# Optimization experiments

Measured on AMD Instinct MI355X. Metric: run time of the kernel, lower is better.

Reference implementation:

```python
import jax, jax.numpy as jnp
import numpy as np

TOP_K = 2
ROUTE_SCALE = 1.0
EPS = 1e-20

B, S, D = 2, 512, 1024
E = 8            # num_experts
F = 768          # moe_intermediate_size
FS = 768 * 1     # shared expert intermediate (moe_intermediate_size * num_shared_experts)


def setup_inputs() -> dict:
    key = jax.random.key(0)
    ks = jax.random.split(key, 9)
    s = 0.02
    return {
        "hidden_states": jax.random.normal(ks[0], (B, S, D), dtype=jnp.float32),
        "W_gate_router": jax.random.normal(ks[1], (D, E), dtype=jnp.float32) * s,
        "expert_bias": jnp.zeros((E,), dtype=jnp.float32),
        "Wg": jax.random.normal(ks[2], (E, D, F), dtype=jnp.float32) * s,
        "Wu": jax.random.normal(ks[3], (E, D, F), dtype=jnp.float32) * s,
        "Wd": jax.random.normal(ks[4], (E, F, D), dtype=jnp.float32) * s,
        "Wg_s": jax.random.normal(ks[5], (D, FS), dtype=jnp.float32) * s,
        "Wu_s": jax.random.normal(ks[6], (D, FS), dtype=jnp.float32) * s,
        "Wd_s": jax.random.normal(ks[7], (FS, D), dtype=jnp.float32) * s,
    }


def reference(hidden_states, W_gate_router, expert_bias, Wg, Wu, Wd, Wg_s, Wu_s, Wd_s):
    b, s, d = hidden_states.shape
    x = hidden_states.reshape(-1, d)                      # [T, D]
    T = x.shape[0]

    # ---- token-choice top-k router (sigmoid scoring, route_norm) ----
    logits = x @ W_gate_router                            # [T, E]
    scores = jax.nn.sigmoid(logits.astype(jnp.float32))   # [T, E] fp32
    _, sel = jax.lax.top_k(scores + expert_bias, TOP_K)   # [T, K] (bias only for selection)
    top_scores = jnp.take_along_axis(scores, sel, axis=1)  # [T, K]
    top_scores = top_scores / (top_scores.sum(-1, keepdims=True) + EPS)  # route_norm
    top_scores = top_scores * ROUTE_SCALE

    # ---- shared expert (always active) ----
    shared = (jax.nn.silu(x @ Wg_s) * (x @ Wu_s)) @ Wd_s  # [T, D]

    # ---- dispatch: N = T*K routed slots (scatter-add is order-independent,
    #      so the torch stable-argsort grouping is mathematically a no-op) ----
    tok = jnp.repeat(jnp.arange(T), TOP_K)                # [N] source token per slot
    exp = sel.reshape(-1)                                 # [N] expert per slot
    w = top_scores.reshape(-1)                            # [N]
    xr = x[tok]                                           # [N, D]

    # per-expert SiLU-GLU MLP, vectorized over experts then select own expert's row
    h = jax.nn.silu(jnp.einsum('nd,edf->enf', xr, Wg)) * jnp.einsum('nd,edf->enf', xr, Wu)
    out_all = jnp.einsum('enf,efd->end', h, Wd)           # [E, N, D]
    routed = out_all[exp, jnp.arange(exp.shape[0])]       # [N, D]
    routed = (routed.astype(jnp.float32) * w[:, None]).astype(hidden_states.dtype)

    # ---- combine: scatter-add routed outputs onto shared output ----
    out = shared.at[tok].add(routed)                      # [T, D]
    return out.reshape(b, s, d)
```

## Files before the change

### kernel.cpp

```cpp
#include <hip/hip_runtime.h>
#include <hip/hip_bf16.h>
#include <math.h>

#define T_TOK   1024
#define D_DIM   1024
#define E_NUM   8
#define F_DIM   768
#define N_SLOTS 2048

typedef unsigned short u16;
typedef __attribute__((ext_vector_type(8))) short bf16x8;
typedef __attribute__((ext_vector_type(4))) float f32x4;

#define WS_SEL    0
#define WS_WTS    8192
#define WS_BUCKET 16384
#define WS_COUNTS 49152
#define WS_OFFS   49216
#define WS_POS    49280
#define WS_XB     65536
#define WS_H      (WS_XB + 2097152)
#define WS_WDT    (WS_H + 4718592)
#define WS_WDST   (WS_WDT + 12582912)
#define WS_WGUT   (WS_WDST + 1572864)
#define WS_WGUST  (WS_WGUT + 25165824)
#define WS_Y      WS_WGUT

__device__ __forceinline__ u16 f2bf(float x) {
    unsigned int u = __float_as_uint(x);
    u += 0x7fffu + ((u >> 16) & 1u);
    return (u16)(u >> 16);
}
__device__ __forceinline__ float bf2f(u16 h) {
    return __uint_as_float(((unsigned int)h) << 16);
}

__device__ __forceinline__ void async16(const void* g, void* s) {
    __builtin_amdgcn_global_load_lds(
        (const __attribute__((address_space(1))) unsigned int*)g,
        (__attribute__((address_space(3))) unsigned int*)s, 16, 0, 0);
}

#define PIN()   __builtin_amdgcn_sched_barrier(0)
#define BAR()   do { PIN(); __builtin_amdgcn_s_barrier(); PIN(); } while (0)
#define WAIT6() do { asm volatile("s_waitcnt vmcnt(6)" ::: "memory"); PIN(); } while (0)
#define WAIT0() do { asm volatile("s_waitcnt vmcnt(0)" ::: "memory"); PIN(); } while (0)

__global__ __launch_bounds__(256) void xrouter_kernel(
    const float* __restrict__ X, const float* __restrict__ Wr,
    const float* __restrict__ bias, u16* __restrict__ Xb,
    int* __restrict__ sel, float* __restrict__ wts)
{
    int t = blockIdx.x * 4 + (threadIdx.x >> 6);
    int lane = threadIdx.x & 63;
    const float* xrow = X + (size_t)t * D_DIM;
    u16* brow = Xb + (size_t)t * D_DIM;
    float acc[E_NUM];
#pragma unroll
    for (int e = 0; e < E_NUM; ++e) acc[e] = 0.f;
#pragma unroll
    for (int q = 0; q < 4; ++q) {
        int d = q * 256 + lane * 4;
        float4 v = *(const float4*)(xrow + d);
        ushort4 o;
        o.x = f2bf(v.x); o.y = f2bf(v.y); o.z = f2bf(v.z); o.w = f2bf(v.w);
        *(ushort4*)(brow + d) = o;
        const float xv[4] = {v.x, v.y, v.z, v.w};
#pragma unroll
        for (int jj = 0; jj < 4; ++jj) {
            const float4* wr = (const float4*)(Wr + (size_t)(d + jj) * E_NUM);
            float4 w0 = wr[0], w1 = wr[1];
            acc[0] += xv[jj] * w0.x; acc[1] += xv[jj] * w0.y;
            acc[2] += xv[jj] * w0.z; acc[3] += xv[jj] * w0.w;
            acc[4] += xv[jj] * w1.x; acc[5] += xv[jj] * w1.y;
            acc[6] += xv[jj] * w1.z; acc[7] += xv[jj] * w1.w;
        }
    }
#pragma unroll
    for (int e = 0; e < E_NUM; ++e)
#pragma unroll
        for (int off = 32; off > 0; off >>= 1)
            acc[e] += __shfl_xor(acc[e], off);
    if (lane == 0) {
        float s[E_NUM], b[E_NUM];
#pragma unroll
        for (int e = 0; e < E_NUM; ++e) {
            s[e] = 1.f / (1.f + expf(-acc[e]));
            b[e] = s[e] + bias[e];
        }
        int i1 = 0; float b1 = b[0];
#pragma unroll
        for (int e = 1; e < E_NUM; ++e) if (b[e] > b1) { b1 = b[e]; i1 = e; }
        int i2 = -1; float b2 = -INFINITY;
#pragma unroll
        for (int e = 0; e < E_NUM; ++e) {
            if (e == i1) continue;
            if (b[e] > b2) { b2 = b[e]; i2 = e; }
        }
        float s1 = s[i1], s2 = s[i2];
        float denom = s1 + s2 + 1e-20f;
        sel[2 * t] = i1; sel[2 * t + 1] = i2;
        wts[2 * t] = s1 / denom; wts[2 * t + 1] = s2 / denom;
    }
}

__global__ __launch_bounds__(512) void dispatch_kernel(
    const int* __restrict__ sel, int* __restrict__ bucket,
    int* __restrict__ counts, int* __restrict__ offs, int* __restrict__ pos)
{
    __shared__ int soffs[E_NUM + 1];
    int e = threadIdx.x >> 6;
    int lane = threadIdx.x & 63;
    int running = 0;
    for (int base = 0; base < N_SLOTS; base += 64) {
        int slot = base + lane;
        bool mine = (sel[slot] == e);
        unsigned long long mask = __ballot(mine);
        if (mine) {
            int rank = running + __popcll(mask & ((1ull << lane) - 1ull));
            bucket[e * T_TOK + rank] = slot;
        }
        running += __popcll(mask);
    }
    if (lane == 0) counts[e] = running;
    __syncthreads();
    if (threadIdx.x == 0) {
        int o = 0;
        for (int k = 0; k < E_NUM; ++k) { soffs[k] = o; offs[k] = o; o += counts[k]; }
        soffs[E_NUM] = o; offs[E_NUM] = o;
    }
    __syncthreads();
    int base_off = soffs[e];
    for (int r = lane; r < running; r += 64)
        pos[bucket[e * T_TOK + r]] = base_off + r;
}

__global__ __launch_bounds__(256) void transpose_cvt(
    const float* __restrict__ Wg, const float* __restrict__ Wu,
    const float* __restrict__ Wd, const float* __restrict__ Wgs,
    const float* __restrict__ Wus, const float* __restrict__ Wds,
    u16* __restrict__ Wgut, u16* __restrict__ Wdt,
    u16* __restrict__ Wgust, u16* __restrict__ Wdst)
{
    int z = blockIdx.z;
    const float* src; u16* dst; int R, C;
    if (z < 8)       { src = Wg + (size_t)z * D_DIM * F_DIM;        dst = Wgut + (size_t)z * 1536 * D_DIM;               R = D_DIM; C = F_DIM; }
    else if (z < 16) { int e = z - 8;  src = Wu + (size_t)e * D_DIM * F_DIM; dst = Wgut + (size_t)e * 1536 * D_DIM + (size_t)F_DIM * D_DIM; R = D_DIM; C = F_DIM; }
    else if (z < 24) { int e = z - 16; src = Wd + (size_t)e * F_DIM * D_DIM; dst = Wdt + (size_t)e * D_DIM * F_DIM;      R = F_DIM; C = D_DIM; }
    else if (z == 24){ src = Wgs; dst = Wgust;                      R = D_DIM; C = F_DIM; }
    else if (z == 25){ src = Wus; dst = Wgust + (size_t)F_DIM * D_DIM; R = D_DIM; C = F_DIM; }
    else             { src = Wds; dst = Wdst;                       R = F_DIM; C = D_DIM; }
    int c0 = blockIdx.x * 64, r0 = blockIdx.y * 64;
    if (c0 >= C || r0 >= R) return;

    __shared__ u16 tile[64][72];
    int t = threadIdx.x;
    int rr = t >> 4, cq = (t & 15) * 4;
#pragma unroll
    for (int i = 0; i < 4; ++i) {
        int rl = rr + 16 * i;
        float4 v = *(const float4*)(src + (size_t)(r0 + rl) * C + c0 + cq);
        tile[cq + 0][rl] = f2bf(v.x);
        tile[cq + 1][rl] = f2bf(v.y);
        tile[cq + 2][rl] = f2bf(v.z);
        tile[cq + 3][rl] = f2bf(v.w);
    }
    __syncthreads();
#pragma unroll
    for (int j = 0; j < 2; ++j) {
        int idx = t + 256 * j;
        int cc = idx >> 3, q = idx & 7;
        *(uint4*)(dst + (size_t)(c0 + cc) * R + r0 + q * 8) = *(const uint4*)&tile[cc][q * 8];
    }
}

__global__ __launch_bounds__(256, 3) void proj1(
    const u16* __restrict__ Xb, const u16* __restrict__ Wgut, const u16* __restrict__ Wgust,
    u16* __restrict__ H,
    const int* __restrict__ bucket, const int* __restrict__ counts, const int* __restrict__ offs)
{
    const int i = blockIdx.x;
    const int cxcd = i & 7, m = i >> 3;
    const int y = m & 31, phi = m >> 5;
    const int panel = phi * 8 + cxcd;
    if (panel >= 108) return;
    const int unit = panel / 12, x = panel - unit * 12;

    int nrows, rbase; const u16* Wt;
    if (unit < E_NUM) {
        nrows = counts[unit]; rbase = offs[unit];
        Wt = Wgut + (size_t)unit * 1536 * D_DIM;
    } else {
        nrows = T_TOK; rbase = N_SLOTS; Wt = Wgust;
    }
    const int row0 = y * 64;
    if (row0 >= nrows) return;

    __shared__ u16 smem[2][192 * 64];

    const int t = threadIdx.x;
    const int wv = t >> 6, lane = t & 63, l15 = lane & 15, lg = lane >> 4;
    const int wm = wv >> 1, wn = wv & 1;
    const int rl = lane >> 3, cch = lane & 7;

    const u16* srcA[2];
#pragma unroll
    for (int j = 0; j < 2; ++j) {
        int arow = wv * 16 + j * 8 + rl;
        int grow = min(row0 + arow, nrows - 1);
        if (unit < E_NUM) grow = bucket[unit * T_TOK + grow] >> 1;
        srcA[j] = Xb + (size_t)grow * D_DIM + (cch ^ (arow & 7)) * 8;
    }
    const u16* srcB[4];
#pragma unroll
    for (int j = 0; j < 4; ++j) {
        int br = wv * 32 + j * 8 + rl;
        size_t n = (size_t)(br >> 6) * F_DIM + x * 64 + (br & 63);
        srcB[j] = Wt + n * D_DIM + (cch ^ (br & 7)) * 8;
    }

    f32x4 accg[2][2], accu[2][2];
    const f32x4 z4 = {0.f, 0.f, 0.f, 0.f};
#pragma unroll
    for (int ri = 0; ri < 2; ++ri)
#pragma unroll
        for (int ci = 0; ci < 2; ++ci) { accg[ri][ci] = z4; accu[ri][ci] = z4; }

#define STAGE1(buf, kt) do { \
    _Pragma("unroll") \
    for (int j = 0; j < 2; ++j) \
        async16(srcA[j] + (kt), &smem[buf][(wv * 16 + j * 8) * 64]); \
    _Pragma("unroll") \
    for (int j = 0; j < 4; ++j) \
        async16(srcB[j] + (kt), &smem[buf][(64 + wv * 32 + j * 8) * 64]); \
} while (0)

#define COMP1(buf) do { \
    bf16x8 av[2][2], bg[2][2], bu[2][2]; \
    _Pragma("unroll") \
    for (int ri = 0; ri < 2; ++ri) { \
        int row = wm * 32 + ri * 16 + l15; \
        _Pragma("unroll") \
        for (int kk = 0; kk < 2; ++kk) { \
            int ch = ((kk << 2) | lg) ^ (row & 7); \
            av[ri][kk] = *(const bf16x8*)&smem[buf][row * 64 + ch * 8]; \
        } \
    } \
    _Pragma("unroll") \
    for (int ci = 0; ci < 2; ++ci) { \
        int br = wn * 32 + ci * 16 + l15; \
        _Pragma("unroll") \
        for (int kk = 0; kk < 2; ++kk) { \
            int ch = ((kk << 2) | lg) ^ (br & 7); \
            bg[ci][kk] = *(const bf16x8*)&smem[buf][(64 + br) * 64 + ch * 8]; \
            bu[ci][kk] = *(const bf16x8*)&smem[buf][(128 + br) * 64 + ch * 8]; \
        } \
    } \
    _Pragma("unroll") \
    for (int kk = 0; kk < 2; ++kk) \
        _Pragma("unroll") \
        for (int ri = 0; ri < 2; ++ri) \
            _Pragma("unroll") \
            for (int ci = 0; ci < 2; ++ci) { \
                accg[ri][ci] = __builtin_amdgcn_mfma_f32_16x16x32_bf16( \
                    av[ri][kk], bg[ci][kk], accg[ri][ci], 0, 0, 0); \
                accu[ri][ci] = __builtin_amdgcn_mfma_f32_16x16x32_bf16( \
                    av[ri][kk], bu[ci][kk], accu[ri][ci], 0, 0, 0); \
            } \
} while (0)

    STAGE1(0, 0);
    for (int tt = 0; tt < 16; tt += 2) {
        STAGE1(1, (tt + 1) * 64);
        WAIT6();
        BAR();
        COMP1(0);
        BAR();
        if (tt + 2 < 16) { STAGE1(0, (tt + 2) * 64); WAIT6(); }
        else             { WAIT0(); }
        BAR();
        COMP1(1);
        BAR();
    }
#undef STAGE1
#undef COMP1

#pragma unroll
    for (int ri = 0; ri < 2; ++ri)
#pragma unroll
        for (int ci = 0; ci < 2; ++ci) {
            int n = x * 64 + wn * 32 + ci * 16 + l15;
#pragma unroll
            for (int r = 0; r < 4; ++r) {
                int row = row0 + wm * 32 + ri * 16 + lg * 4 + r;
                if (row >= nrows) continue;
                float gv = accg[ri][ci][r];
                float uv = accu[ri][ci][r];
                H[(size_t)(rbase + row) * F_DIM + n] =
                    f2bf(gv / (1.f + __expf(-gv)) * uv);
            }
        }
}

__global__ __launch_bounds__(256, 3) void proj2(
    const u16* __restrict__ H, const u16* __restrict__ Wdt, const u16* __restrict__ Wdst,
    float* __restrict__ Y,
    const int* __restrict__ counts, const int* __restrict__ offs)
{
    const int i = blockIdx.x;
    const int cxcd = i & 7, m = i >> 3;
    const int y = m & 31, phi = m >> 5;
    const int panel = phi * 8 + cxcd;
    const int unit = panel >> 3, x = panel & 7;

    int nrows, rbase; const u16* Wt;
    if (unit < E_NUM) {
        nrows = counts[unit]; rbase = offs[unit];
        Wt = Wdt + (size_t)unit * D_DIM * F_DIM;
    } else {
        nrows = T_TOK; rbase = N_SLOTS; Wt = Wdst;
    }
    const int row0 = y * 64, n0 = x * 128;
    if (row0 >= nrows) return;

    __shared__ u16 smem[2][192 * 64];

    const int t = threadIdx.x;
    const int wv = t >> 6, lane = t & 63, l15 = lane & 15, lg = lane >> 4;
    const int wm = wv >> 1, wn = wv & 1;
    const int rl = lane >> 3, cch = lane & 7;

    const u16* srcA[2];
#pragma unroll
    for (int j = 0; j < 2; ++j) {
        int arow = wv * 16 + j * 8 + rl;
        int grow = rbase + min(row0 + arow, nrows - 1);
        srcA[j] = H + (size_t)grow * F_DIM + (cch ^ (arow & 7)) * 8;
    }
    const u16* srcB[4];
#pragma unroll
    for (int j = 0; j < 4; ++j) {
        int br = wv * 32 + j * 8 + rl;
        srcB[j] = Wt + (size_t)(n0 + br) * F_DIM + (cch ^ (br & 7)) * 8;
    }

    f32x4 acc[2][4];
    const f32x4 z4 = {0.f, 0.f, 0.f, 0.f};
#pragma unroll
    for (int ri = 0; ri < 2; ++ri)
#pragma unroll
        for (int ci = 0; ci < 4; ++ci) acc[ri][ci] = z4;

#define STAGE2(buf, kt) do { \
    _Pragma("unroll") \
    for (int j = 0; j < 2; ++j) \
        async16(srcA[j] + (kt), &smem[buf][(wv * 16 + j * 8) * 64]); \
    _Pragma("unroll") \
    for (int j = 0; j < 4; ++j) \
        async16(srcB[j] + (kt), &smem[buf][(64 + wv * 32 + j * 8) * 64]); \
} while (0)

#define COMP2(buf) do { \
    bf16x8 av[2][2], bv[4][2]; \
    _Pragma("unroll") \
    for (int ri = 0; ri < 2; ++ri) { \
        int row = wm * 32 + ri * 16 + l15; \
        _Pragma("unroll") \
        for (int kk = 0; kk < 2; ++kk) { \
            int ch = ((kk << 2) | lg) ^ (row & 7); \
            av[ri][kk] = *(const bf16x8*)&smem[buf][row * 64 + ch * 8]; \
        } \
    } \
    _Pragma("unroll") \
    for (int ci = 0; ci < 4; ++ci) { \
        int br = wn * 64 + ci * 16 + l15; \
        _Pragma("unroll") \
        for (int kk = 0; kk < 2; ++kk) { \
            int ch = ((kk << 2) | lg) ^ (br & 7); \
            bv[ci][kk] = *(const bf16x8*)&smem[buf][(64 + br) * 64 + ch * 8]; \
        } \
    } \
    _Pragma("unroll") \
    for (int kk = 0; kk < 2; ++kk) \
        _Pragma("unroll") \
        for (int ri = 0; ri < 2; ++ri) \
            _Pragma("unroll") \
            for (int ci = 0; ci < 4; ++ci) \
                acc[ri][ci] = __builtin_amdgcn_mfma_f32_16x16x32_bf16( \
                    av[ri][kk], bv[ci][kk], acc[ri][ci], 0, 0, 0); \
} while (0)

    STAGE2(0, 0);
    for (int tt = 0; tt < 12; tt += 2) {
        STAGE2(1, (tt + 1) * 64);
        WAIT6();
        BAR();
        COMP2(0);
        BAR();
        if (tt + 2 < 12) { STAGE2(0, (tt + 2) * 64); WAIT6(); }
        else             { WAIT0(); }
        BAR();
        COMP2(1);
        BAR();
    }
#undef STAGE2
#undef COMP2

#pragma unroll
    for (int ri = 0; ri < 2; ++ri)
#pragma unroll
        for (int ci = 0; ci < 4; ++ci) {
            int n = n0 + wn * 64 + ci * 16 + l15;
#pragma unroll
            for (int r = 0; r < 4; ++r) {
                int row = row0 + wm * 32 + ri * 16 + lg * 4 + r;
                if (row >= nrows) continue;
                Y[(size_t)(rbase + row) * D_DIM + n] = acc[ri][ci][r];
            }
        }
}

__global__ __launch_bounds__(256) void combine_kernel(
    const float* __restrict__ Y, const int* __restrict__ pos,
    const float* __restrict__ wts, float* __restrict__ out)
{
    int t = blockIdx.x;
    int d = threadIdx.x * 4;
    int p0 = pos[2 * t], p1 = pos[2 * t + 1];
    float w0 = wts[2 * t], w1 = wts[2 * t + 1];
    float4 a = *(const float4*)(Y + (size_t)(N_SLOTS + t) * D_DIM + d);
    float4 b = *(const float4*)(Y + (size_t)p0 * D_DIM + d);
    float4 cc = *(const float4*)(Y + (size_t)p1 * D_DIM + d);
    float4 o;
    o.x = a.x + w0 * b.x + w1 * cc.x;
    o.y = a.y + w0 * b.y + w1 * cc.y;
    o.z = a.z + w0 * b.z + w1 * cc.z;
    o.w = a.w + w0 * b.w + w1 * cc.w;
    *(float4*)(out + (size_t)t * D_DIM + d) = o;
}

extern "C" void kernel_launch(void* const* d_in, const int* in_sizes, int n_in,
                              void* d_out, int out_size, void* d_ws, size_t ws_size,
                              hipStream_t stream) {
    const float* X    = (const float*)d_in[0];
    const float* Wr   = (const float*)d_in[1];
    const float* bias = (const float*)d_in[2];
    const float* Wg   = (const float*)d_in[3];
    const float* Wu   = (const float*)d_in[4];
    const float* Wd   = (const float*)d_in[5];
    const float* Wgs  = (const float*)d_in[6];
    const float* Wus  = (const float*)d_in[7];
    const float* Wds  = (const float*)d_in[8];
    float* out = (float*)d_out;

    char* ws = (char*)d_ws;
    int*   sel    = (int*)(ws + WS_SEL);
    float* wtsv   = (float*)(ws + WS_WTS);
    int*   bucket = (int*)(ws + WS_BUCKET);
    int*   counts = (int*)(ws + WS_COUNTS);
    int*   offs   = (int*)(ws + WS_OFFS);
    int*   pos    = (int*)(ws + WS_POS);
    u16*   Xb     = (u16*)(ws + WS_XB);
    u16*   H      = (u16*)(ws + WS_H);
    u16*   Wdt    = (u16*)(ws + WS_WDT);
    u16*   Wdst   = (u16*)(ws + WS_WDST);
    u16*   Wgut   = (u16*)(ws + WS_WGUT);
    u16*   Wgust  = (u16*)(ws + WS_WGUST);
    float* Y      = (float*)(ws + WS_Y);

    xrouter_kernel<<<256, 256, 0, stream>>>(X, Wr, bias, Xb, sel, wtsv);
    dispatch_kernel<<<1, 512, 0, stream>>>(sel, bucket, counts, offs, pos);
    transpose_cvt<<<dim3(16, 16, 27), 256, 0, stream>>>(
        Wg, Wu, Wd, Wgs, Wus, Wds, Wgut, Wdt, Wgust, Wdst);

    proj1<<<3584, 256, 0, stream>>>(Xb, Wgut, Wgust, H, bucket, counts, offs);
    proj2<<<2304, 256, 0, stream>>>(H, Wdt, Wdst, Y, counts, offs);
    combine_kernel<<<T_TOK, 256, 0, stream>>>(Y, pos, wtsv, out);
}
```

Before: 85.31 us.

## Fuse weight transposes into router and proj1 kernels to overlap work

```diff
diff --git a/kernel.cpp b/kernel.cpp
--- a/kernel.cpp
+++ b/kernel.cpp
@@ -46,12 +46,53 @@
 #define WAIT6() do { asm volatile("s_waitcnt vmcnt(6)" ::: "memory"); PIN(); } while (0)
 #define WAIT0() do { asm volatile("s_waitcnt vmcnt(0)" ::: "memory"); PIN(); } while (0)
 
-__global__ __launch_bounds__(256) void xrouter_kernel(
+__device__ __forceinline__ void tr_tile(
+    const float* __restrict__ src, u16* __restrict__ dst,
+    int R, int C, int r0, int c0, u16 (*tile)[72])
+{
+    int t = threadIdx.x;
+    int rr = t >> 4, cq = (t & 15) * 4;
+#pragma unroll
+    for (int i = 0; i < 4; ++i) {
+        int rl = rr + 16 * i;
+        float4 v = *(const float4*)(src + (size_t)(r0 + rl) * C + c0 + cq);
+        tile[cq + 0][rl] = f2bf(v.x);
+        tile[cq + 1][rl] = f2bf(v.y);
+        tile[cq + 2][rl] = f2bf(v.z);
+        tile[cq + 3][rl] = f2bf(v.w);
+    }
+    __syncthreads();
+#pragma unroll
+    for (int j = 0; j < 2; ++j) {
+        int idx = t + 256 * j;
+        int cc = idx >> 3, q = idx & 7;
+        *(uint4*)(dst + (size_t)(c0 + cc) * R + r0 + q * 8) = *(const uint4*)&tile[cc][q * 8];
+    }
+}
+
+__global__ __launch_bounds__(256) void prep1_kernel(
     const float* __restrict__ X, const float* __restrict__ Wr,
-    const float* __restrict__ bias, u16* __restrict__ Xb,
-    int* __restrict__ sel, float* __restrict__ wts)
-{
-    int t = blockIdx.x * 4 + (threadIdx.x >> 6);
+    const float* __restrict__ bias,
+    const float* __restrict__ Wg, const float* __restrict__ Wu,
+    const float* __restrict__ Wgs, const float* __restrict__ Wus,
+    u16* __restrict__ Xb, int* __restrict__ sel, float* __restrict__ wts,
+    u16* __restrict__ Wgut, u16* __restrict__ Wgust)
+{
+    const int i = blockIdx.x;
+    if (i < 3456) {
+        __shared__ u16 tile[64][72];
+        const int z = i / 192;
+        const int rem = i - z * 192;
+        const int rtile = rem / 12, ctile = rem - rtile * 12;
+        const float* src; u16* dst;
+        if (z < 8)       { src = Wg + (size_t)z * D_DIM * F_DIM;       dst = Wgut + (size_t)z * 1536 * D_DIM; }
+        else if (z < 16) { src = Wu + (size_t)(z - 8) * D_DIM * F_DIM; dst = Wgut + (size_t)(z - 8) * 1536 * D_DIM + (size_t)F_DIM * D_DIM; }
+        else if (z == 16){ src = Wgs; dst = Wgust; }
+        else             { src = Wus; dst = Wgust + (size_t)F_DIM * D_DIM; }
+        tr_tile(src, dst, D_DIM, F_DIM, rtile * 64, ctile * 64, tile);
+        return;
+    }
+    int t = (i - 3456) * 4 + (threadIdx.x >> 6);
     int lane = threadIdx.x & 63;
     const float* xrow = X + (size_t)t * D_DIM;
     u16* brow = Xb + (size_t)t * D_DIM;
@@ -135,51 +176,27 @@
         pos[bucket[e * T_TOK + r]] = base_off + r;
 }
 
-__global__ __launch_bounds__(256) void transpose_cvt(
-    const float* __restrict__ Wg, const float* __restrict__ Wu,
-    const float* __restrict__ Wd, const float* __restrict__ Wgs,
-    const float* __restrict__ Wus, const float* __restrict__ Wds,
-    u16* __restrict__ Wgut, u16* __restrict__ Wdt,
-    u16* __restrict__ Wgust, u16* __restrict__ Wdst)
-{
-    int z = blockIdx.z;
-    const float* src; u16* dst; int R, C;
-    if (z < 8)       { src = Wg + (size_t)z * D_DIM * F_DIM;        dst = Wgut + (size_t)z * 1536 * D_DIM;               R = D_DIM; C = F_DIM; }
-    else if (z < 16) { int e = z - 8;  src = Wu + (size_t)e * D_DIM * F_DIM; dst = Wgut + (size_t)e * 1536 * D_DIM + (size_t)F_DIM * D_DIM; R = D_DIM; C = F_DIM; }
-    else if (z < 24) { int e = z - 16; src = Wd + (size_t)e * F_DIM * D_DIM; dst = Wdt + (size_t)e * D_DIM * F_DIM;      R = F_DIM; C = D_DIM; }
-    else if (z == 24){ src = Wgs; dst = Wgust;                      R = D_DIM; C = F_DIM; }
-    else if (z == 25){ src = Wus; dst = Wgust + (size_t)F_DIM * D_DIM; R = D_DIM; C = F_DIM; }
-    else             { src = Wds; dst = Wdst;                       R = F_DIM; C = D_DIM; }
-    int c0 = blockIdx.x * 64, r0 = blockIdx.y * 64;
-    if (c0 >= C || r0 >= R) return;
-
-    __shared__ u16 tile[64][72];
-    int t = threadIdx.x;
-    int rr = t >> 4, cq = (t & 15) * 4;
-#pragma unroll
-    for (int i = 0; i < 4; ++i) {
-        int rl = rr + 16 * i;
-        float4 v = *(const float4*)(src + (size_t)(r0 + rl) * C + c0 + cq);
-        tile[cq + 0][rl] = f2bf(v.x);
-        tile[cq + 1][rl] = f2bf(v.y);
-        tile[cq + 2][rl] = f2bf(v.z);
-        tile[cq + 3][rl] = f2bf(v.w);
-    }
-    __syncthreads();
-#pragma unroll
-    for (int j = 0; j < 2; ++j) {
-        int idx = t + 256 * j;
-        int cc = idx >> 3, q = idx & 7;
-        *(uint4*)(dst + (size_t)(c0 + cc) * R + r0 + q * 8) = *(const uint4*)&tile[cc][q * 8];
-    }
-}
-
-__global__ __launch_bounds__(256, 3) void proj1(
+__global__ __launch_bounds__(256, 3) void proj1_fused(
     const u16* __restrict__ Xb, const u16* __restrict__ Wgut, const u16* __restrict__ Wgust,
     u16* __restrict__ H,
-    const int* __restrict__ bucket, const int* __restrict__ counts, const int* __restrict__ offs)
-{
+    const int* __restrict__ bucket, const int* __restrict__ counts, const int* __restrict__ offs,
+    const float* __restrict__ Wd, const float* __restrict__ Wds,
+    u16* __restrict__ Wdt, u16* __restrict__ Wdst)
+{
+    __shared__ u16 smem[2][192 * 64];
     const int i = blockIdx.x;
+    if (i >= 3584) {
+        const int j = i - 3584;
+        const int z = j / 192;
+        const int rem = j - z * 192;
+        const int rtile = rem >> 4, ctile = rem & 15;
+        const float* src; u16* dst;
+        if (z < 8) { src = Wd + (size_t)z * F_DIM * D_DIM; dst = Wdt + (size_t)z * D_DIM * F_DIM; }
+        else       { src = Wds; dst = Wdst; }
+        tr_tile(src, dst, F_DIM, D_DIM, rtile * 64, ctile * 64, (u16(*)[72])&smem[0][0]);
+        return;
+    }
+
     const int cxcd = i & 7, m = i >> 3;
     const int y = m & 31, phi = m >> 5;
     const int panel = phi * 8 + cxcd;
@@ -195,8 +212,6 @@
     }
     const int row0 = y * 64;
     if (row0 >= nrows) return;
-
-    __shared__ u16 smem[2][192 * 64];
 
     const int t = threadIdx.x;
     const int wv = t >> 6, lane = t & 63, l15 = lane & 15, lg = lane >> 4;
@@ -468,12 +483,12 @@
     u16*   Wgust  = (u16*)(ws + WS_WGUST);
     float* Y      = (float*)(ws + WS_Y);
 
-    xrouter_kernel<<<256, 256, 0, stream>>>(X, Wr, bias, Xb, sel, wtsv);
+    prep1_kernel<<<3712, 256, 0, stream>>>(
+        X, Wr, bias, Wg, Wu, Wgs, Wus, Xb, sel, wtsv, Wgut, Wgust);
     dispatch_kernel<<<1, 512, 0, stream>>>(sel, bucket, counts, offs, pos);
-    transpose_cvt<<<dim3(16, 16, 27), 256, 0, stream>>>(
-        Wg, Wu, Wd, Wgs, Wus, Wds, Wgut, Wdt, Wgust, Wdst);
-
-    proj1<<<3584, 256, 0, stream>>>(Xb, Wgut, Wgust, H, bucket, counts, offs);
+
+    proj1_fused<<<5312, 256, 0, stream>>>(
+        Xb, Wgut, Wgust, H, bucket, counts, offs, Wd, Wds, Wdt, Wdst);
     proj2<<<2304, 256, 0, stream>>>(H, Wdt, Wdst, Y, counts, offs);
     combine_kernel<<<T_TOK, 256, 0, stream>>>(Y, pos, wtsv, out);
 }
```

After: 87.03 us. 2.0% more time.

## Fuse fp32 weight conversion into GEMM loads, dropping separate transpose kernel

Applied to the files above, without the earlier changes.

```diff
diff --git a/kernel.cpp b/kernel.cpp
--- a/kernel.cpp
+++ b/kernel.cpp
@@ -9,6 +9,7 @@
 #define N_SLOTS 2048
 
 typedef unsigned short u16;
+typedef unsigned int   u32;
 typedef __attribute__((ext_vector_type(8))) short bf16x8;
 typedef __attribute__((ext_vector_type(4))) float f32x4;
 
@@ -20,20 +21,14 @@
 #define WS_POS    49280
 #define WS_XB     65536
 #define WS_H      (WS_XB + 2097152)
-#define WS_WDT    (WS_H + 4718592)
-#define WS_WDST   (WS_WDT + 12582912)
-#define WS_WGUT   (WS_WDST + 1572864)
-#define WS_WGUST  (WS_WGUT + 25165824)
-#define WS_Y      WS_WGUT
+#define WS_Y      (WS_H + 4718592)
 
 __device__ __forceinline__ u16 f2bf(float x) {
-    unsigned int u = __float_as_uint(x);
+    u32 u = __float_as_uint(x);
     u += 0x7fffu + ((u >> 16) & 1u);
     return (u16)(u >> 16);
 }
-__device__ __forceinline__ float bf2f(u16 h) {
-    return __uint_as_float(((unsigned int)h) << 16);
-}
+#define PKBF(hi, lo) __builtin_amdgcn_perm(__float_as_uint(hi), __float_as_uint(lo), 0x07060302u)
 
 __device__ __forceinline__ void async16(const void* g, void* s) {
     __builtin_amdgcn_global_load_lds(
@@ -41,10 +36,10 @@
         (__attribute__((address_space(3))) unsigned int*)s, 16, 0, 0);
 }
 
-#define PIN()   __builtin_amdgcn_sched_barrier(0)
-#define BAR()   do { PIN(); __builtin_amdgcn_s_barrier(); PIN(); } while (0)
-#define WAIT6() do { asm volatile("s_waitcnt vmcnt(6)" ::: "memory"); PIN(); } while (0)
-#define WAIT0() do { asm volatile("s_waitcnt vmcnt(0)" ::: "memory"); PIN(); } while (0)
+#define PIN()    __builtin_amdgcn_sched_barrier(0)
+#define BAR()    do { PIN(); __builtin_amdgcn_s_barrier(); PIN(); } while (0)
+#define WAITV(n) do { asm volatile("s_waitcnt vmcnt(" #n ")" ::: "memory"); PIN(); } while (0)
+#define LGKM0()  do { asm volatile("s_waitcnt lgkmcnt(0)" ::: "memory"); PIN(); } while (0)
 
 __global__ __launch_bounds__(256) void xrouter_kernel(
     const float* __restrict__ X, const float* __restrict__ Wr,
@@ -135,47 +130,10 @@
         pos[bucket[e * T_TOK + r]] = base_off + r;
 }
 
-__global__ __launch_bounds__(256) void transpose_cvt(
+__global__ __launch_bounds__(256, 2) void proj1(
+    const u16* __restrict__ Xb,
     const float* __restrict__ Wg, const float* __restrict__ Wu,
-    const float* __restrict__ Wd, const float* __restrict__ Wgs,
-    const float* __restrict__ Wus, const float* __restrict__ Wds,
-    u16* __restrict__ Wgut, u16* __restrict__ Wdt,
-    u16* __restrict__ Wgust, u16* __restrict__ Wdst)
-{
-    int z = blockIdx.z;
-    const float* src; u16* dst; int R, C;
-    if (z < 8)       { src = Wg + (size_t)z * D_DIM * F_DIM;        dst = Wgut + (size_t)z * 1536 * D_DIM;               R = D_DIM; C = F_DIM; }
-    else if (z < 16) { int e = z - 8;  src = Wu + (size_t)e * D_DIM * F_DIM; dst = Wgut + (size_t)e * 1536 * D_DIM + (size_t)F_DIM * D_DIM; R = D_DIM; C = F_DIM; }
-    else if (z < 24) { int e = z - 16; src = Wd + (size_t)e * F_DIM * D_DIM; dst = Wdt + (size_t)e * D_DIM * F_DIM;      R = F_DIM; C = D_DIM; }
-    else if (z == 24){ src = Wgs; dst = Wgust;                      R = D_DIM; C = F_DIM; }
-    else if (z == 25){ src = Wus; dst = Wgust + (size_t)F_DIM * D_DIM; R = D_DIM; C = F_DIM; }
-    else             { src = Wds; dst = Wdst;                       R = F_DIM; C = D_DIM; }
-    int c0 = blockIdx.x * 64, r0 = blockIdx.y * 64;
-    if (c0 >= C || r0 >= R) return;
-
-    __shared__ u16 tile[64][72];
-    int t = threadIdx.x;
-    int rr = t >> 4, cq = (t & 15) * 4;
-#pragma unroll
-    for (int i = 0; i < 4; ++i) {
-        int rl = rr + 16 * i;
-        float4 v = *(const float4*)(src + (size_t)(r0 + rl) * C + c0 + cq);
-        tile[cq + 0][rl] = f2bf(v.x);
-        tile[cq + 1][rl] = f2bf(v.y);
-        tile[cq + 2][rl] = f2bf(v.z);
-        tile[cq + 3][rl] = f2bf(v.w);
-    }
-    __syncthreads();
-#pragma unroll
-    for (int j = 0; j < 2; ++j) {
-        int idx = t + 256 * j;
-        int cc = idx >> 3, q = idx & 7;
-        *(uint4*)(dst + (size_t)(c0 + cc) * R + r0 + q * 8) = *(const uint4*)&tile[cc][q * 8];
-    }
-}
-
-__global__ __launch_bounds__(256, 3) void proj1(
-    const u16* __restrict__ Xb, const u16* __restrict__ Wgut, const u16* __restrict__ Wgust,
+    const float* __restrict__ Wgs, const float* __restrict__ Wus,
     u16* __restrict__ H,
     const int* __restrict__ bucket, const int* __restrict__ counts, const int* __restrict__ offs)
 {
@@ -186,37 +144,44 @@
     if (panel >= 108) return;
     const int unit = panel / 12, x = panel - unit * 12;
 
-    int nrows, rbase; const u16* Wt;
+    int nrows, rbase; const float *Bg, *Bu;
     if (unit < E_NUM) {
         nrows = counts[unit]; rbase = offs[unit];
-        Wt = Wgut + (size_t)unit * 1536 * D_DIM;
-    } else {
-        nrows = T_TOK; rbase = N_SLOTS; Wt = Wgust;
-    }
+        Bg = Wg + (size_t)unit * D_DIM * F_DIM;
+        Bu = Wu + (size_t)unit * D_DIM * F_DIM;
+    } else { nrows = T_TOK; rbase = N_SLOTS; Bg = Wgs; Bu = Wus; }
     const int row0 = y * 64;
     if (row0 >= nrows) return;
 
-    __shared__ u16 smem[2][192 * 64];
+    __shared__ u16 smem[3][6144];
 
     const int t = threadIdx.x;
-    const int wv = t >> 6, lane = t & 63, l15 = lane & 15, lg = lane >> 4;
+    const int wv = t >> 6, lane = t & 63, l15 = lane & 15;
     const int wm = wv >> 1, wn = wv & 1;
-    const int rl = lane >> 3, cch = lane & 7;
-
-    const u16* srcA[2];
-#pragma unroll
-    for (int j = 0; j < 2; ++j) {
-        int arow = wv * 16 + j * 8 + rl;
-        int grow = min(row0 + arow, nrows - 1);
-        if (unit < E_NUM) grow = bucket[unit * T_TOK + grow] >> 1;
-        srcA[j] = Xb + (size_t)grow * D_DIM + (cch ^ (arow & 7)) * 8;
-    }
-    const u16* srcB[4];
-#pragma unroll
-    for (int j = 0; j < 4; ++j) {
-        int br = wv * 32 + j * 8 + rl;
-        size_t n = (size_t)(br >> 6) * F_DIM + x * 64 + (br & 63);
-        srcB[j] = Wt + n * D_DIM + (cch ^ (br & 7)) * 8;
+
+    int arow = 16 * wv + (lane >> 2);
+    int grow = min(row0 + arow, nrows - 1);
+    if (unit < E_NUM) grow = bucket[unit * T_TOK + grow] >> 1;
+    const int fA = ((lane >> 2) & 3) ^ ((lane >> 4) & 1);
+    const u16* srcA = Xb + (size_t)grow * D_DIM + ((lane & 3) ^ fA) * 8;
+
+    const int ngrp = t & 31, kgrp = t >> 5;
+    const int n0 = 4 * ngrp, k0 = 4 * kgrp;
+    const float* srcB = ((n0 < 64) ? Bg : Bu) + (size_t)k0 * F_DIM + x * 64 + (n0 & 63);
+    const int wch  = (kgrp >> 1) ^ (ngrp & 3);
+    const int woff = 2048 + n0 * 32 + wch * 8 + (kgrp & 1) * 4;
+
+    const int g4  = lane >> 4;
+    const int chA = g4 ^ (l15 & 3) ^ ((l15 >> 2) & 1);
+    const int chB = g4 ^ ((l15 >> 2) & 3);
+    int offA[2], offG[2], offU[2];
+#pragma unroll
+    for (int ri = 0; ri < 2; ++ri)
+        offA[ri] = (wm * 32 + ri * 16 + l15) * 32 + chA * 8;
+#pragma unroll
+    for (int ci = 0; ci < 2; ++ci) {
+        offG[ci] = 2048 + (wn * 32 + ci * 16 + l15) * 32 + chB * 8;
+        offU[ci] = offG[ci] + 64 * 32;
     }
 
     f32x4 accg[2][2], accu[2][2];
@@ -226,65 +191,68 @@
 #pragma unroll
         for (int ci = 0; ci < 2; ++ci) { accg[ri][ci] = z4; accu[ri][ci] = z4; }
 
-#define STAGE1(buf, kt) do { \
+    float4 SA[4], SB[4];
+#define LOADB1(SV, tile) do { \
+    const float* _s = srcB + (size_t)((tile) * 32) * F_DIM; \
+    SV[0] = *(const float4*)(_s);             _s += F_DIM; \
+    SV[1] = *(const float4*)(_s);             _s += F_DIM; \
+    SV[2] = *(const float4*)(_s);             _s += F_DIM; \
+    SV[3] = *(const float4*)(_s); } while (0)
+#define WRITEB1(SV, buf) do { \
+    u16* _bb = smem[(buf)]; \
+    const float* _f0 = (const float*)&SV[0]; const float* _f1 = (const float*)&SV[1]; \
+    const float* _f2 = (const float*)&SV[2]; const float* _f3 = (const float*)&SV[3]; \
     _Pragma("unroll") \
-    for (int j = 0; j < 2; ++j) \
-        async16(srcA[j] + (kt), &smem[buf][(wv * 16 + j * 8) * 64]); \
-    _Pragma("unroll") \
-    for (int j = 0; j < 4; ++j) \
-        async16(srcB[j] + (kt), &smem[buf][(64 + wv * 32 + j * 8) * 64]); \
+    for (int j = 0; j < 4; ++j) { \
+        u32 _w0 = PKBF(_f1[j], _f0[j]); \
+        u32 _w1 = PKBF(_f3[j], _f2[j]); \
+        *(uint2*)&_bb[woff + j * 32] = make_uint2(_w0, _w1); \
+    } } while (0)
+#define COMP1(buf) do { \
+    const u16* _p = smem[(buf)]; \
+    bf16x8 _av[2], _bg[2], _bu[2]; \
+    _Pragma("unroll") for (int ri = 0; ri < 2; ++ri) _av[ri] = *(const bf16x8*)&_p[offA[ri]]; \
+    _Pragma("unroll") for (int ci = 0; ci < 2; ++ci) { \
+        _bg[ci] = *(const bf16x8*)&_p[offG[ci]]; \
+        _bu[ci] = *(const bf16x8*)&_p[offU[ci]]; } \
+    _Pragma("unroll") for (int ri = 0; ri < 2; ++ri) \
+        _Pragma("unroll") for (int ci = 0; ci < 2; ++ci) { \
+            accg[ri][ci] = __builtin_amdgcn_mfma_f32_16x16x32_bf16(_av[ri], _bg[ci], accg[ri][ci], 0, 0, 0); \
+            accu[ri][ci] = __builtin_amdgcn_mfma_f32_16x16x32_bf16(_av[ri], _bu[ci], accu[ri][ci], 0, 0, 0); } \
+    } while (0)
+#define BODY1(tt, SV) do { \
+    WAITV(6); \
+    WRITEB1(SV, ((tt) + 2) % 3); \
+    LOADB1(SV, min((tt) + 4, 31)); \
+    LGKM0(); \
+    BAR(); \
+    COMP1((tt) % 3); \
+    BAR(); \
+    async16(srcA + min((tt) + 3, 31) * 32, &smem[(tt) % 3][wv * 512]); \
 } while (0)
 
-#define COMP1(buf) do { \
-    bf16x8 av[2][2], bg[2][2], bu[2][2]; \
-    _Pragma("unroll") \
-    for (int ri = 0; ri < 2; ++ri) { \
-        int row = wm * 32 + ri * 16 + l15; \
-        _Pragma("unroll") \
-        for (int kk = 0; kk < 2; ++kk) { \
-            int ch = ((kk << 2) | lg) ^ (row & 7); \
-            av[ri][kk] = *(const bf16x8*)&smem[buf][row * 64 + ch * 8]; \
-        } \
-    } \
-    _Pragma("unroll") \
-    for (int ci = 0; ci < 2; ++ci) { \
-        int br = wn * 32 + ci * 16 + l15; \
-        _Pragma("unroll") \
-        for (int kk = 0; kk < 2; ++kk) { \
-            int ch = ((kk << 2) | lg) ^ (br & 7); \
-            bg[ci][kk] = *(const bf16x8*)&smem[buf][(64 + br) * 64 + ch * 8]; \
-            bu[ci][kk] = *(const bf16x8*)&smem[buf][(128 + br) * 64 + ch * 8]; \
-        } \
-    } \
-    _Pragma("unroll") \
-    for (int kk = 0; kk < 2; ++kk) \
-        _Pragma("unroll") \
-        for (int ri = 0; ri < 2; ++ri) \
-            _Pragma("unroll") \
-            for (int ci = 0; ci < 2; ++ci) { \
-                accg[ri][ci] = __builtin_amdgcn_mfma_f32_16x16x32_bf16( \
-                    av[ri][kk], bg[ci][kk], accg[ri][ci], 0, 0, 0); \
-                accu[ri][ci] = __builtin_amdgcn_mfma_f32_16x16x32_bf16( \
-                    av[ri][kk], bu[ci][kk], accu[ri][ci], 0, 0, 0); \
-            } \
-} while (0)
-
-    STAGE1(0, 0);
-    for (int tt = 0; tt < 16; tt += 2) {
-        STAGE1(1, (tt + 1) * 64);
-        WAIT6();
-        BAR();
-        COMP1(0);
-        BAR();
-        if (tt + 2 < 16) { STAGE1(0, (tt + 2) * 64); WAIT6(); }
-        else             { WAIT0(); }
-        BAR();
-        COMP1(1);
-        BAR();
-    }
-#undef STAGE1
+    LOADB1(SA, 0);
+    LOADB1(SB, 1);
+    WAITV(4);
+    WRITEB1(SA, 0);
+    async16(srcA, &smem[0][wv * 512]);
+    LOADB1(SA, 2);
+    WAITV(5);
+    WRITEB1(SB, 1);
+    async16(srcA + 32, &smem[1][wv * 512]);
+    LOADB1(SB, 3);
+    async16(srcA + 64, &smem[2][wv * 512]);
+
+    for (int tt = 0; tt < 32; tt += 2) {
+        BODY1(tt, SA);
+        BODY1(tt + 1, SB);
+    }
+#undef BODY1
 #undef COMP1
-
+#undef WRITEB1
+#undef LOADB1
+
+    const int lg = lane >> 4;
 #pragma unroll
     for (int ri = 0; ri < 2; ++ri)
 #pragma unroll
@@ -302,8 +270,9 @@
         }
 }
 
-__global__ __launch_bounds__(256, 3) void proj2(
-    const u16* __restrict__ H, const u16* __restrict__ Wdt, const u16* __restrict__ Wdst,
+__global__ __launch_bounds__(256, 2) void proj2(
+    const u16* __restrict__ H,
+    const float* __restrict__ Wd, const float* __restrict__ Wds,
     float* __restrict__ Y,
     const int* __restrict__ counts, const int* __restrict__ offs)
 {
@@ -311,106 +280,111 @@
     const int cxcd = i & 7, m = i >> 3;
     const int y = m & 31, phi = m >> 5;
     const int panel = phi * 8 + cxcd;
-    const int unit = panel >> 3, x = panel & 7;
-
-    int nrows, rbase; const u16* Wt;
+    const int unit = panel >> 4, x = panel & 15;
+
+    int nrows, rbase; const float* Bm;
     if (unit < E_NUM) {
         nrows = counts[unit]; rbase = offs[unit];
-        Wt = Wdt + (size_t)unit * D_DIM * F_DIM;
-    } else {
-        nrows = T_TOK; rbase = N_SLOTS; Wt = Wdst;
-    }
-    const int row0 = y * 64, n0 = x * 128;
+        Bm = Wd + (size_t)unit * F_DIM * D_DIM;
+    } else { nrows = T_TOK; rbase = N_SLOTS; Bm = Wds; }
+    const int row0 = y * 64;
     if (row0 >= nrows) return;
 
-    __shared__ u16 smem[2][192 * 64];
+    __shared__ u16 smem[3][4096];
 
     const int t = threadIdx.x;
-    const int wv = t >> 6, lane = t & 63, l15 = lane & 15, lg = lane >> 4;
+    const int wv = t >> 6, lane = t & 63, l15 = lane & 15;
     const int wm = wv >> 1, wn = wv & 1;
-    const int rl = lane >> 3, cch = lane & 7;
-
-    const u16* srcA[2];
-#pragma unroll
-    for (int j = 0; j < 2; ++j) {
-        int arow = wv * 16 + j * 8 + rl;
-        int grow = rbase + min(row0 + arow, nrows - 1);
-        srcA[j] = H + (size_t)grow * F_DIM + (cch ^ (arow & 7)) * 8;
-    }
-    const u16* srcB[4];
-#pragma unroll
-    for (int j = 0; j < 4; ++j) {
-        int br = wv * 32 + j * 8 + rl;
-        srcB[j] = Wt + (size_t)(n0 + br) * F_DIM + (cch ^ (br & 7)) * 8;
-    }
-
-    f32x4 acc[2][4];
+
+    int arow = 16 * wv + (lane >> 2);
+    int grow = rbase + min(row0 + arow, nrows - 1);
+    const int fA = ((lane >> 2) & 3) ^ ((lane >> 4) & 1);
+    const u16* srcA = H + (size_t)grow * F_DIM + ((lane & 3) ^ fA) * 8;
+
+    const int ngrp = t & 15, kgrp = t >> 4;
+    const int n0 = 4 * ngrp, k0 = 2 * kgrp;
+    const float* srcB = Bm + (size_t)k0 * D_DIM + x * 64 + n0;
+    const int wch  = (k0 >> 3) ^ (ngrp & 3);
+    const int woff = 2048 + n0 * 32 + wch * 8 + (k0 & 7);
+
+    const int g4  = lane >> 4;
+    const int chA = g4 ^ (l15 & 3) ^ ((l15 >> 2) & 1);
+    const int chB = g4 ^ ((l15 >> 2) & 3);
+    int offA[2], offB[2];
+#pragma unroll
+    for (int ri = 0; ri < 2; ++ri)
+        offA[ri] = (wm * 32 + ri * 16 + l15) * 32 + chA * 8;
+#pragma unroll
+    for (int ci = 0; ci < 2; ++ci)
+        offB[ci] = 2048 + (wn * 32 + ci * 16 + l15) * 32 + chB * 8;
+
+    f32x4 acc[2][2];
     const f32x4 z4 = {0.f, 0.f, 0.f, 0.f};
 #pragma unroll
     for (int ri = 0; ri < 2; ++ri)
 #pragma unroll
-        for (int ci = 0; ci < 4; ++ci) acc[ri][ci] = z4;
-
-#define STAGE2(buf, kt) do { \
+        for (int ci = 0; ci < 2; ++ci) acc[ri][ci] = z4;
+
+    float4 SA[2], SB[2];
+#define LOADB2(SV, tile) do { \
+    const float* _s = srcB + (size_t)((tile) * 32) * D_DIM; \
+    SV[0] = *(const float4*)(_s); \
+    SV[1] = *(const float4*)(_s + D_DIM); } while (0)
+#define WRITEB2(SV, buf) do { \
+    u16* _bb = smem[(buf)]; \
+    const float* _f0 = (const float*)&SV[0]; const float* _f1 = (const float*)&SV[1]; \
     _Pragma("unroll") \
-    for (int j = 0; j < 2; ++j) \
-        async16(srcA[j] + (kt), &smem[buf][(wv * 16 + j * 8) * 64]); \
-    _Pragma("unroll") \
-    for (int j = 0; j < 4; ++j) \
-        async16(srcB[j] + (kt), &smem[buf][(64 + wv * 32 + j * 8) * 64]); \
+    for (int j = 0; j < 4; ++j) { \
+        u32 _w = PKBF(_f1[j], _f0[j]); \
+        *(u32*)&_bb[woff + j * 32] = _w; \
+    } } while (0)
+#define COMP2(buf) do { \
+    const u16* _p = smem[(buf)]; \
+    bf16x8 _av[2], _bv[2]; \
+    _Pragma("unroll") for (int ri = 0; ri < 2; ++ri) _av[ri] = *(const bf16x8*)&_p[offA[ri]]; \
+    _Pragma("unroll") for (int ci = 0; ci < 2; ++ci) _bv[ci] = *(const bf16x8*)&_p[offB[ci]]; \
+    _Pragma("unroll") for (int ri = 0; ri < 2; ++ri) \
+        _Pragma("unroll") for (int ci = 0; ci < 2; ++ci) \
+            acc[ri][ci] = __builtin_amdgcn_mfma_f32_16x16x32_bf16(_av[ri], _bv[ci], acc[ri][ci], 0, 0, 0); \
+    } while (0)
+#define BODY2(tt, SV) do { \
+    WAITV(4); \
+    WRITEB2(SV, ((tt) + 2) % 3); \
+    LOADB2(SV, min((tt) + 4, 23)); \
+    LGKM0(); \
+    BAR(); \
+    COMP2((tt) % 3); \
+    BAR(); \
+    async16(srcA + min((tt) + 3, 23) * 32, &smem[(tt) % 3][wv * 512]); \
 } while (0)
 
-#define COMP2(buf) do { \
-    bf16x8 av[2][2], bv[4][2]; \
-    _Pragma("unroll") \
-    for (int ri = 0; ri < 2; ++ri) { \
-        int row = wm * 32 + ri * 16 + l15; \
-        _Pragma("unroll") \
-        for (int kk = 0; kk < 2; ++kk) { \
-            int ch = ((kk << 2) | lg) ^ (row & 7); \
-            av[ri][kk] = *(const bf16x8*)&smem[buf][row * 64 + ch * 8]; \
-        } \
-    } \
-    _Pragma("unroll") \
-    for (int ci = 0; ci < 4; ++ci) { \
-        int br = wn * 64 + ci * 16 + l15; \
-        _Pragma("unroll") \
-        for (int kk = 0; kk < 2; ++kk) { \
-            int ch = ((kk << 2) | lg) ^ (br & 7); \
-            bv[ci][kk] = *(const bf16x8*)&smem[buf][(64 + br) * 64 + ch * 8]; \
-        } \
-    } \
-    _Pragma("unroll") \
-    for (int kk = 0; kk < 2; ++kk) \
-        _Pragma("unroll") \
-        for (int ri = 0; ri < 2; ++ri) \
-            _Pragma("unroll") \
-            for (int ci = 0; ci < 4; ++ci) \
-                acc[ri][ci] = __builtin_amdgcn_mfma_f32_16x16x32_bf16( \
-                    av[ri][kk], bv[ci][kk], acc[ri][ci], 0, 0, 0); \
-} while (0)
-
-    STAGE2(0, 0);
-    for (int tt = 0; tt < 12; tt += 2) {
-        STAGE2(1, (tt + 1) * 64);
-        WAIT6();
-        BAR();
-        COMP2(0);
-        BAR();
-        if (tt + 2 < 12) { STAGE2(0, (tt + 2) * 64); WAIT6(); }
-        else             { WAIT0(); }
-        BAR();
-        COMP2(1);
-        BAR();
-    }
-#undef STAGE2
+    LOADB2(SA, 0);
+    LOADB2(SB, 1);
+    WAITV(2);
+    WRITEB2(SA, 0);
+    async16(srcA, &smem[0][wv * 512]);
+    LOADB2(SA, 2);
+    WAITV(3);
+    WRITEB2(SB, 1);
+    async16(srcA + 32, &smem[1][wv * 512]);
+    LOADB2(SB, 3);
+    async16(srcA + 64, &smem[2][wv * 512]);
+
+    for (int tt = 0; tt < 24; tt += 2) {
+        BODY2(tt, SA);
+        BODY2(tt + 1, SB);
+    }
+#undef BODY2
 #undef COMP2
-
-#pragma unroll
-    for (int ri = 0; ri < 2; ++ri)
-#pragma unroll
-        for (int ci = 0; ci < 4; ++ci) {
-            int n = n0 + wn * 64 + ci * 16 + l15;
+#undef WRITEB2
+#undef LOADB2
+
+    const int lg = lane >> 4;
+#pragma unroll
+    for (int ri = 0; ri < 2; ++ri)
+#pragma unroll
+        for (int ci = 0; ci < 2; ++ci) {
+            int n = x * 64 + wn * 32 + ci * 16 + l15;
 #pragma unroll
             for (int r = 0; r < 4; ++r) {
                 int row = row0 + wm * 32 + ri * 16 + lg * 4 + r;
@@ -462,18 +436,12 @@
     int*   pos    = (int*)(ws + WS_POS);
     u16*   Xb     = (u16*)(ws + WS_XB);
     u16*   H      = (u16*)(ws + WS_H);
-    u16*   Wdt    = (u16*)(ws + WS_WDT);
-    u16*   Wdst   = (u16*)(ws + WS_WDST);
-    u16*   Wgut   = (u16*)(ws + WS_WGUT);
-    u16*   Wgust  = (u16*)(ws + WS_WGUST);
     float* Y      = (float*)(ws + WS_Y);
 
     xrouter_kernel<<<256, 256, 0, stream>>>(X, Wr, bias, Xb, sel, wtsv);
     dispatch_kernel<<<1, 512, 0, stream>>>(sel, bucket, counts, offs, pos);
-    transpose_cvt<<<dim3(16, 16, 27), 256, 0, stream>>>(
-        Wg, Wu, Wd, Wgs, Wus, Wds, Wgut, Wdt, Wgust, Wdst);
-
-    proj1<<<3584, 256, 0, stream>>>(Xb, Wgut, Wgust, H, bucket, counts, offs);
-    proj2<<<2304, 256, 0, stream>>>(H, Wdt, Wdst, Y, counts, offs);
+
+    proj1<<<3584, 256, 0, stream>>>(Xb, Wg, Wu, Wgs, Wus, H, bucket, counts, offs);
+    proj2<<<4608, 256, 0, stream>>>(H, Wd, Wds, Y, counts, offs);
     combine_kernel<<<T_TOK, 256, 0, stream>>>(Y, pos, wtsv, out);
 }
```

Result: slower. 99.83 us (+17.0%).
